# Kernel tuning notes

Hardware: AMD Instinct MI355X
Metric: run time of the kernel (lower is better)

The kernel has to match this reference:

```python
import jax, jax.numpy as jnp
import numpy as np

N = 100000   # nodes
F = 32       # input features
D = 64       # dim_inner
E = 1600000  # edges
G = 2000     # graphs
C = 10       # classes
L = 4        # GIN layers
BN_EPS = 1e-5


def _bn(h, gamma, beta):
    # training-mode BatchNorm1d over node axis (biased variance, as torch)
    mu = jnp.mean(h, axis=0)
    var = jnp.mean((h - mu) ** 2, axis=0)
    return gamma * (h - mu) * jax.lax.rsqrt(var + BN_EPS) + beta


def setup_inputs() -> dict:
    key = jax.random.key(0)
    ks = jax.random.split(key, 24)
    s = 0.05
    f32 = jnp.float32
    x = jax.random.normal(ks[0], (N, F), f32)
    edge_index = jax.random.randint(ks[1], (2, E), 0, N)
    batch_ids = jnp.sort(jax.random.randint(ks[2], (N,), 0, G))
    y = jax.random.randint(ks[3], (G,), 0, C)
    W_enc = jax.random.normal(ks[4], (F, D), f32) * s
    b_enc = jnp.zeros((D,), f32)
    W1 = jax.random.normal(ks[5], (L, D, D), f32) * s
    b1 = jnp.zeros((L, D), f32)
    g1 = jnp.ones((L, D), f32)
    be1 = jnp.zeros((L, D), f32)
    W2 = jax.random.normal(ks[6], (L, D, D), f32) * s
    b2 = jnp.zeros((L, D), f32)
    gout = jnp.ones((L, D), f32)
    bout = jnp.zeros((L, D), f32)
    fcW0 = jax.random.normal(ks[7], (F, C), f32) * s
    fcb0 = jnp.zeros((C,), f32)
    fcW = jax.random.normal(ks[8], (L, D, C), f32) * s
    fcb = jnp.zeros((L, C), f32)
    return dict(x=x, edge_index=edge_index, batch_ids=batch_ids, y=y,
                W_enc=W_enc, b_enc=b_enc, W1=W1, b1=b1, g1=g1, be1=be1,
                W2=W2, b2=b2, gout=gout, bout=bout,
                fcW0=fcW0, fcb0=fcb0, fcW=fcW, fcb=fcb)


def reference(x, edge_index, batch_ids, y, W_enc, b_enc, W1, b1, g1, be1,
              W2, b2, gout, bout, fcW0, fcb0, fcW, fcb):
    src, dst = edge_index[0], edge_index[1]
    h = x @ W_enc + b_enc  # x_encoder
    layer_outs = []
    for i in range(L):
        # GINConv, eps=0: (1+eps)*x + sum_{j->i} x_j  (scatter-add over edges)
        agg = jax.ops.segment_sum(h[src], dst, num_segments=N)
        m = h + agg
        m = jax.nn.relu(_bn(m @ W1[i] + b1[i], g1[i], be1[i]))  # MLP part 1
        m = m @ W2[i] + b2[i]                                    # MLP part 2
        h = jax.nn.relu(_bn(m, gout[i], bout[i]))                # outer BN+ReLU
        layer_outs.append(h)
    # jumping-knowledge: pooled raw features + each layer through its fc head
    out = jax.ops.segment_sum(x, batch_ids, num_segments=G) @ fcW0 + fcb0
    for i in range(L):
        pooled = jax.ops.segment_sum(layer_outs[i], batch_ids, num_segments=G)
        out = out + pooled @ fcW[i] + fcb[i]
    return (out, y)
```

## Files before the change

### kernel.cpp

```cpp
#include <hip/hip_runtime.h>


#define BN_EPS 1e-5f
#define CURS_STRIDE 16

typedef __attribute__((ext_vector_type(8))) short short8;
typedef __attribute__((ext_vector_type(4))) float f32x4;

__device__ __forceinline__ unsigned int pack_bf16x2(float a, float b) {
    unsigned int ua = __float_as_uint(a);
    unsigned int ub = __float_as_uint(b);
    ua = (ua + 0x7FFFu + ((ua >> 16) & 1u)) >> 16;
    ub = (ub + 0x7FFFu + ((ub >> 16) & 1u)) >> 16;
    return ua | (ub << 16);
}
__device__ __forceinline__ unsigned short bf16_1(float f) {
    unsigned int u = __float_as_uint(f);
    u = (u + 0x7FFFu + ((u >> 16) & 1u)) >> 16;
    return (unsigned short)u;
}
__device__ __forceinline__ float2 unpack_bf16x2(unsigned int u) {
    float2 r;
    r.x = __uint_as_float(u << 16);
    r.y = __uint_as_float(u & 0xFFFF0000u);
    return r;
}

template<bool BN>
__device__ __forceinline__ void acc_row8(float (&acc)[8], uint4 p,
                                         const float* sc, const float* sh) {
    unsigned int pp[4] = {p.x, p.y, p.z, p.w};
    #pragma unroll
    for (int t = 0; t < 4; t++) {
        float2 f = unpack_bf16x2(pp[t]);
        if (BN) {
            f.x = fmaxf(fmaf(f.x, sc[2 * t],     sh[2 * t]),     0.f);
            f.y = fmaxf(fmaf(f.y, sc[2 * t + 1], sh[2 * t + 1]), 0.f);
        }
        acc[2 * t]     += f.x;
        acc[2 * t + 1] += f.y;
    }
}

template<bool BN>
__global__ __launch_bounds__(512)
void gin_gemm1(const int* __restrict__ rowp, const int* __restrict__ srcs,
               const unsigned int* __restrict__ hb,
               const float* __restrict__ bsum, const float* __restrict__ bsumsq,
               const float* __restrict__ gamma, const float* __restrict__ beta,
               float invN,
               const float* __restrict__ W, const float* __restrict__ bias,
               unsigned short* __restrict__ out,
               float* __restrict__ stat_sum, float* __restrict__ stat_sumsq,
               int N)
{
    constexpr int AS = 72, WS = 72, KH = 2;
    __shared__ short a_lds[128 * AS];
    __shared__ short wt_lds[64 * WS];
    __shared__ float ssf[128];
    __shared__ float red[1024];

    const int tid = threadIdx.x;
    const int nb  = blockIdx.x * 128;
    const int l   = tid & 63;
    const int w   = tid >> 6;
    const int ln  = l & 15;
    const int q   = l >> 4;

    if (BN) {
        if (tid < 64) {
            float mu  = bsum[tid] * invN;
            float var = bsumsq[tid] * invN - mu * mu;
            float s   = gamma[tid] * rsqrtf(var + BN_EPS);
            ssf[tid]      = s;
            ssf[64 + tid] = beta[tid] - s * mu;
        }
        __syncthreads();
    }

    for (int idx = tid; idx < 64 * 64; idx += 512) {
        int k = idx >> 6, n = idx & 63;
        wt_lds[n * WS + k] = (short)bf16_1(W[idx]);
    }

    const uint4* hb4 = (const uint4*)hb;
    const int cc = tid & 7;
    const int rl = tid >> 3;
    float sc[8], sh[8];
    if (BN) {
        #pragma unroll
        for (int j = 0; j < 8; j++) {
            sc[j] = ssf[cc * 8 + j];
            sh[j] = ssf[64 + cc * 8 + j];
        }
    }
    for (int it = 0; it < 2; it++) {
        int rloc = it * 64 + rl;
        int n = nb + rloc;
        float acc[8] = {0.f, 0.f, 0.f, 0.f, 0.f, 0.f, 0.f, 0.f};
        if (n < N) {
            uint4 p = hb4[(size_t)n * 8 + cc];
            acc_row8<BN>(acc, p, sc, sh);
            int e = rowp[n], end = rowp[n + 1];
            for (; e + 3 < end; e += 4) {
                int a0 = srcs[e], a1 = srcs[e + 1], a2 = srcs[e + 2], a3 = srcs[e + 3];
                uint4 p0 = hb4[(size_t)a0 * 8 + cc];
                uint4 p1 = hb4[(size_t)a1 * 8 + cc];
                uint4 p2 = hb4[(size_t)a2 * 8 + cc];
                uint4 p3 = hb4[(size_t)a3 * 8 + cc];
                acc_row8<BN>(acc, p0, sc, sh);
                acc_row8<BN>(acc, p1, sc, sh);
                acc_row8<BN>(acc, p2, sc, sh);
                acc_row8<BN>(acc, p3, sc, sh);
            }
            for (; e < end; e++) {
                uint4 pp = hb4[(size_t)srcs[e] * 8 + cc];
                acc_row8<BN>(acc, pp, sc, sh);
            }
        }
        uint4 o;
        o.x = pack_bf16x2(acc[0], acc[1]);
        o.y = pack_bf16x2(acc[2], acc[3]);
        o.z = pack_bf16x2(acc[4], acc[5]);
        o.w = pack_bf16x2(acc[6], acc[7]);
        *(uint4*)&a_lds[rloc * AS + cc * 8] = o;
    }
    __syncthreads();

    short8 afrag[KH], bfrag[4][KH];
    const int rw = w * 16;
    #pragma unroll
    for (int kh = 0; kh < KH; kh++)
        afrag[kh] = *(const short8*)&a_lds[(rw + ln) * AS + kh * 32 + q * 8];
    #pragma unroll
    for (int nt = 0; nt < 4; nt++)
        #pragma unroll
        for (int kh = 0; kh < KH; kh++)
            bfrag[nt][kh] = *(const short8*)&wt_lds[(nt * 16 + ln) * WS + kh * 32 + q * 8];

    f32x4 acc[4];
    #pragma unroll
    for (int nt = 0; nt < 4; nt++) {
        float bv = bias[nt * 16 + ln];
        acc[nt] = (f32x4){bv, bv, bv, bv};
    }
    #pragma unroll
    for (int kh = 0; kh < KH; kh++)
        #pragma unroll
        for (int nt = 0; nt < 4; nt++)
            acc[nt] = __builtin_amdgcn_mfma_f32_16x16x32_bf16(
                afrag[kh], bfrag[nt][kh], acc[nt], 0, 0, 0);

    #pragma unroll
    for (int reg = 0; reg < 4; reg++) {
        int row = nb + rw + q * 4 + reg;
        if (row < N)
            #pragma unroll
            for (int nt = 0; nt < 4; nt++)
                out[(size_t)row * 64 + nt * 16 + ln] = bf16_1(acc[nt][reg]);
    }

    {
        float s1[4] = {0.f, 0.f, 0.f, 0.f};
        float s2[4] = {0.f, 0.f, 0.f, 0.f};
        #pragma unroll
        for (int reg = 0; reg < 4; reg++) {
            int row = nb + rw + q * 4 + reg;
            if (row < N)
                #pragma unroll
                for (int nt = 0; nt < 4; nt++) {
                    float v = acc[nt][reg];
                    s1[nt] += v;
                    s2[nt] += v * v;
                }
        }
        #pragma unroll
        for (int nt = 0; nt < 4; nt++) {
            s1[nt] += __shfl_xor(s1[nt], 16);
            s1[nt] += __shfl_xor(s1[nt], 32);
            s2[nt] += __shfl_xor(s2[nt], 16);
            s2[nt] += __shfl_xor(s2[nt], 32);
        }
        __syncthreads();
        if (l < 16) {
            #pragma unroll
            for (int nt = 0; nt < 4; nt++) {
                red[w * 64 + nt * 16 + l]        = s1[nt];
                red[512 + w * 64 + nt * 16 + l]  = s2[nt];
            }
        }
        __syncthreads();
        if (tid < 64) {
            float t1 = 0.f, t2 = 0.f;
            #pragma unroll
            for (int j = 0; j < 8; j++) {
                t1 += red[j * 64 + tid];
                t2 += red[512 + j * 64 + tid];
            }
            unsafeAtomicAdd(&stat_sum[tid],   t1);
            unsafeAtomicAdd(&stat_sumsq[tid], t2);
        }
    }
}

template<int K, int INK, bool STATS>
__global__ __launch_bounds__(512)
void mfma_gemm(const void* __restrict__ Av,
               const float* __restrict__ bn_sum, const float* __restrict__ bn_sumsq,
               const float* __restrict__ gamma, const float* __restrict__ beta,
               float invN,
               const float* __restrict__ W, const float* __restrict__ bias,
               unsigned short* __restrict__ out,
               float* __restrict__ stat_sum, float* __restrict__ stat_sumsq,
               int N)
{
    constexpr int AS  = K + 8;
    constexpr int WS  = K + 8;
    constexpr int CPR = K / 8;
    constexpr int KH  = K / 32;

    __shared__ short a_lds[128 * AS];
    __shared__ short wt_lds[64 * WS];
    __shared__ float ssf[128];
    __shared__ float red[1024];

    const int tid = threadIdx.x;
    const int nb  = blockIdx.x * 128;
    const int l   = tid & 63;
    const int w   = tid >> 6;
    const int ln  = l & 15;
    const int q   = l >> 4;

    if (INK == 2) {
        if (tid < 64) {
            float mu  = bn_sum[tid] * invN;
            float var = bn_sumsq[tid] * invN - mu * mu;
            float s   = gamma[tid] * rsqrtf(var + BN_EPS);
            ssf[tid]      = s;
            ssf[64 + tid] = beta[tid] - s * mu;
        }
        __syncthreads();
    }

    for (int idx = tid; idx < K * 64; idx += 512) {
        int k = idx >> 6, n = idx & 63;
        wt_lds[n * WS + k] = (short)bf16_1(W[idx]);
    }

    for (int c = tid; c < 128 * CPR; c += 512) {
        int rloc = c / CPR;
        int j    = c % CPR;
        int row  = nb + rloc;
        uint4 p = make_uint4(0u, 0u, 0u, 0u);
        if (row < N) {
            if (INK == 1) {
                const float4* xr = (const float4*)Av;
                float4 f0 = xr[(size_t)row * (K / 4) + 2 * j];
                float4 f1 = xr[(size_t)row * (K / 4) + 2 * j + 1];
                p.x = pack_bf16x2(f0.x, f0.y); p.y = pack_bf16x2(f0.z, f0.w);
                p.z = pack_bf16x2(f1.x, f1.y); p.w = pack_bf16x2(f1.z, f1.w);
            } else {
                p = ((const uint4*)Av)[(size_t)row * CPR + j];
                if (INK == 2) {
                    int k0 = j * 8;
                    unsigned int* pp = (unsigned int*)&p;
                    #pragma unroll
                    for (int t = 0; t < 4; t++) {
                        float2 f = unpack_bf16x2(pp[t]);
                        int k = k0 + 2 * t;
                        f.x = fmaxf(fmaf(f.x, ssf[k],     ssf[64 + k]),     0.f);
                        f.y = fmaxf(fmaf(f.y, ssf[k + 1], ssf[64 + k + 1]), 0.f);
                        pp[t] = pack_bf16x2(f.x, f.y);
                    }
                }
            }
        }
        *(uint4*)&a_lds[rloc * AS + j * 8] = p;
    }
    __syncthreads();

    short8 afrag[KH], bfrag[4][KH];
    const int rw = w * 16;
    #pragma unroll
    for (int kh = 0; kh < KH; kh++)
        afrag[kh] = *(const short8*)&a_lds[(rw + ln) * AS + kh * 32 + q * 8];
    #pragma unroll
    for (int nt = 0; nt < 4; nt++)
        #pragma unroll
        for (int kh = 0; kh < KH; kh++)
            bfrag[nt][kh] = *(const short8*)&wt_lds[(nt * 16 + ln) * WS + kh * 32 + q * 8];

    f32x4 acc[4];
    #pragma unroll
    for (int nt = 0; nt < 4; nt++) {
        float bv = bias[nt * 16 + ln];
        acc[nt] = (f32x4){bv, bv, bv, bv};
    }
    #pragma unroll
    for (int kh = 0; kh < KH; kh++)
        #pragma unroll
        for (int nt = 0; nt < 4; nt++)
            acc[nt] = __builtin_amdgcn_mfma_f32_16x16x32_bf16(
                afrag[kh], bfrag[nt][kh], acc[nt], 0, 0, 0);

    #pragma unroll
    for (int reg = 0; reg < 4; reg++) {
        int row = nb + rw + q * 4 + reg;
        if (row < N)
            #pragma unroll
            for (int nt = 0; nt < 4; nt++)
                out[(size_t)row * 64 + nt * 16 + ln] = bf16_1(acc[nt][reg]);
    }

    if (STATS) {
        float s1[4] = {0.f, 0.f, 0.f, 0.f};
        float s2[4] = {0.f, 0.f, 0.f, 0.f};
        #pragma unroll
        for (int reg = 0; reg < 4; reg++) {
            int row = nb + rw + q * 4 + reg;
            if (row < N)
                #pragma unroll
                for (int nt = 0; nt < 4; nt++) {
                    float v = acc[nt][reg];
                    s1[nt] += v;
                    s2[nt] += v * v;
                }
        }
        #pragma unroll
        for (int nt = 0; nt < 4; nt++) {
            s1[nt] += __shfl_xor(s1[nt], 16);
            s1[nt] += __shfl_xor(s1[nt], 32);
            s2[nt] += __shfl_xor(s2[nt], 16);
            s2[nt] += __shfl_xor(s2[nt], 32);
        }
        __syncthreads();
        if (l < 16) {
            #pragma unroll
            for (int nt = 0; nt < 4; nt++) {
                red[w * 64 + nt * 16 + l]       = s1[nt];
                red[512 + w * 64 + nt * 16 + l] = s2[nt];
            }
        }
        __syncthreads();
        if (tid < 64) {
            float t1 = 0.f, t2 = 0.f;
            #pragma unroll
            for (int j = 0; j < 8; j++) {
                t1 += red[j * 64 + tid];
                t2 += red[512 + j * 64 + tid];
            }
            unsafeAtomicAdd(&stat_sum[tid],   t1);
            unsafeAtomicAdd(&stat_sumsq[tid], t2);
        }
    }
}

__global__ __launch_bounds__(256)
void bucket_hist(const int* __restrict__ dst, int* __restrict__ bhist,
                 int E, int nb)
{
    __shared__ int lh[1024];
    for (int i = threadIdx.x; i < 1024; i += 256) lh[i] = 0;
    __syncthreads();
    for (int e = blockIdx.x * 256 + threadIdx.x; e < E; e += gridDim.x * 256)
        atomicAdd(&lh[dst[e] >> 7], 1);
    __syncthreads();
    for (int i = threadIdx.x; i < nb; i += 256)
        if (lh[i]) atomicAdd(&bhist[i], lh[i]);
}

__global__ __launch_bounds__(1024)
void bucket_scan(const int* __restrict__ bhist, int* __restrict__ bbase,
                 int* __restrict__ bcur, int nb)
{
    __shared__ int sm[1024];
    int t = threadIdx.x;
    int v = (t < nb) ? bhist[t] : 0;
    sm[t] = v; __syncthreads();
    for (int off = 1; off < 1024; off <<= 1) {
        int add = (t >= off) ? sm[t - off] : 0;
        __syncthreads();
        sm[t] += add;
        __syncthreads();
    }
    if (t <= nb) {
        int ex = sm[t] - v;
        bbase[t] = ex;
        if (t < nb) bcur[t * CURS_STRIDE] = ex;
    }
}

__global__ __launch_bounds__(256)
void bucket_scatter(const int* __restrict__ src, const int* __restrict__ dst,
                    int* __restrict__ bcur, int* __restrict__ ebuf,
                    int E, int nb)
{
    constexpr int CH = 4096;
    __shared__ int            key[CH];
    __shared__ unsigned short bid[CH];
    __shared__ int lh[800];
    __shared__ int lbase[800];

    const int t    = threadIdx.x;
    const int base = blockIdx.x * CH;
    const int cnt  = min(CH, E - base);

    for (int i = t; i < nb; i += 256) lh[i] = 0;
    __syncthreads();

    for (int i = t; i < cnt; i += 256) {
        int d = dst[base + i];
        int s = src[base + i];
        int b = d >> 7;
        key[i] = (s << 7) | (d & 127);
        bid[i] = (unsigned short)b;
        atomicAdd(&lh[b], 1);
    }
    __syncthreads();

    for (int i = t; i < nb; i += 256) {
        int c = lh[i];
        if (c) lbase[i] = atomicAdd(&bcur[i * CURS_STRIDE], c);
        lh[i] = 0;
    }
    __syncthreads();

    for (int i = t; i < cnt; i += 256) {
        int b = bid[i];
        int p = atomicAdd(&lh[b], 1);
        ebuf[lbase[b] + p] = key[i];
    }
}

__global__ __launch_bounds__(256)
void bucket_csr(const int* __restrict__ bbase, const int* __restrict__ ebuf,
                int* __restrict__ row, int* __restrict__ srcs, int N, int E)
{
    __shared__ int lh[128], lofs[128], lcur[128];
    const int b   = blockIdx.x;
    const int tid = threadIdx.x;
    const int beg = bbase[b], end = bbase[b + 1];

    if (tid < 128) lh[tid] = 0;
    __syncthreads();
    for (int e = beg + tid; e < end; e += 256)
        atomicAdd(&lh[ebuf[e] & 127], 1);
    __syncthreads();

    int v = (tid < 128) ? lh[tid] : 0;
    if (tid < 128) lofs[tid] = v;
    __syncthreads();
    for (int off = 1; off < 128; off <<= 1) {
        int add = 0;
        if (tid < 128 && tid >= off) add = lofs[tid - off];
        __syncthreads();
        if (tid < 128) lofs[tid] += add;
        __syncthreads();
    }
    if (tid < 128) {
        int ex = lofs[tid] - v;
        lcur[tid] = ex;
        int node = b * 128 + tid;
        if (node < N) row[node] = beg + ex;
    }
    if (b == 0 && tid == 0) row[N] = E;
    __syncthreads();

    for (int e = beg + tid; e < end; e += 256) {
        int pk = ebuf[e];
        int p = atomicAdd(&lcur[pk & 127], 1);
        srcs[beg + p] = pk >> 7;
    }
}

__global__ __launch_bounds__(256)
void pool_nodes(const unsigned short* __restrict__ hb,
                const float* __restrict__ bsum, const float* __restrict__ bsumsq,
                const float* __restrict__ gamma, const float* __restrict__ beta,
                float invN, const int* __restrict__ batch,
                float* __restrict__ pooled, int N)
{
    int d  = threadIdx.x & 63;
    int nl = threadIdx.x >> 6;
    int nb = blockIdx.x * 32;
    float mu  = bsum[d] * invN;
    float var = bsumsq[d] * invN - mu * mu;
    float s   = gamma[d] * rsqrtf(var + BN_EPS);
    float sh  = beta[d] - s * mu;
    float acc = 0.f;
    int cg = -1;
    #pragma unroll
    for (int r = 0; r < 8; r++) {
        int n = nb + nl * 8 + r;
        if (n >= N) break;
        int g = batch[n];
        if (g != cg) {
            if (cg >= 0) unsafeAtomicAdd(&pooled[(size_t)cg * 64 + d], acc);
            acc = 0.f; cg = g;
        }
        float v = __uint_as_float(((unsigned int)hb[(size_t)n * 64 + d]) << 16);
        acc += fmaxf(fmaf(v, s, sh), 0.f);
    }
    if (cg >= 0) unsafeAtomicAdd(&pooled[(size_t)cg * 64 + d], acc);
}

__global__ __launch_bounds__(256)
void pool_x(const float* __restrict__ x, const int* __restrict__ batch,
            float* __restrict__ px, int N)
{
    int f  = threadIdx.x & 31;
    int nl = threadIdx.x >> 5;
    int nb = blockIdx.x * 64;
    float acc = 0.f;
    int cg = -1;
    #pragma unroll
    for (int r = 0; r < 8; r++) {
        int n = nb + nl * 8 + r;
        if (n >= N) break;
        int g = batch[n];
        if (g != cg) {
            if (cg >= 0) unsafeAtomicAdd(&px[(size_t)cg * 32 + f], acc);
            acc = 0.f; cg = g;
        }
        acc += x[(size_t)n * 32 + f];
    }
    if (cg >= 0) unsafeAtomicAdd(&px[(size_t)cg * 32 + f], acc);
}

__global__ __launch_bounds__(256)
void head_kernel(const float* __restrict__ px, const float* __restrict__ pl,
                 const float* __restrict__ fcW0, const float* __restrict__ fcb0,
                 const float* __restrict__ fcW, const float* __restrict__ fcb,
                 const int* __restrict__ y, float* __restrict__ out, int G)
{
    int tid = blockIdx.x * 256 + threadIdx.x;
    int total = G * 10;
    if (tid < total) {
        int g = tid / 10, c = tid % 10;
        float acc = fcb0[c];
        const float* pxg = px + (size_t)g * 32;
        #pragma unroll
        for (int k = 0; k < 32; k++) acc = fmaf(pxg[k], fcW0[k * 10 + c], acc);
        #pragma unroll
        for (int i = 0; i < 4; i++) {
            acc += fcb[i * 10 + c];
            const float* pg = pl + ((size_t)i * G + g) * 64;
            const float* w  = fcW + i * 640;
            #pragma unroll
            for (int k = 0; k < 64; k++) acc = fmaf(pg[k], w[k * 10 + c], acc);
        }
        out[tid] = acc;
    } else if (tid < total + G) {
        out[tid] = (float)y[tid - total];
    }
}

extern "C" void kernel_launch(void* const* d_in, const int* in_sizes, int n_in,
                              void* d_out, int out_size, void* d_ws, size_t ws_size,
                              hipStream_t stream)
{
    const float* x     = (const float*)d_in[0];
    const int*   ei    = (const int*)  d_in[1];
    const int*   batch = (const int*)  d_in[2];
    const int*   y     = (const int*)  d_in[3];
    const float* W_enc = (const float*)d_in[4];
    const float* b_enc = (const float*)d_in[5];
    const float* W1    = (const float*)d_in[6];
    const float* b1    = (const float*)d_in[7];
    const float* g1    = (const float*)d_in[8];
    const float* be1   = (const float*)d_in[9];
    const float* W2    = (const float*)d_in[10];
    const float* b2    = (const float*)d_in[11];
    const float* gout  = (const float*)d_in[12];
    const float* bout  = (const float*)d_in[13];
    const float* fcW0  = (const float*)d_in[14];
    const float* fcb0  = (const float*)d_in[15];
    const float* fcW   = (const float*)d_in[16];
    const float* fcb   = (const float*)d_in[17];

    const int N = in_sizes[0] / 32;
    const int E = in_sizes[1] / 2;
    const int G = in_sizes[3];
    const int* src = ei;
    const int* dst = ei + E;
    const int NB = (N + 127) / 128;

    unsigned int* m  = (unsigned int*)d_ws;
    unsigned int* hb = m + (size_t)N * 32;
    float* stats = (float*)(hb + (size_t)N * 32);
    float* px    = stats + 1024;
    float* pl    = px + (size_t)G * 32;
    int*   row   = (int*)(pl + (size_t)4 * G * 64);
    int*   srcs  = row + (N + 1);
    int*   mi    = (int*)m;
    int*   bhist = mi;
    int*   bbase = mi + 1024;
    int*   bcur  = mi + 2048;
    int*   ebuf  = mi + 2048 + 800 * CURS_STRIDE;

    size_t zbytes = (size_t)(1024 + G * 32 + 4 * G * 64) * sizeof(float);
    hipMemsetAsync(stats, 0, zbytes, stream);
    hipMemsetAsync(bhist, 0, 1024 * sizeof(int), stream);

    bucket_hist<<<160, 256, 0, stream>>>(dst, bhist, E, NB);
    bucket_scan<<<1, 1024, 0, stream>>>(bhist, bbase, bcur, NB);
    bucket_scatter<<<(E + 4095) / 4096, 256, 0, stream>>>(src, dst, bcur, ebuf, E, NB);
    bucket_csr<<<NB, 256, 0, stream>>>(bbase, ebuf, row, srcs, N, E);

    const int gb = (N + 127) / 128;
    const float invN = 1.0f / (float)N;

    mfma_gemm<32, 1, false><<<gb, 512, 0, stream>>>(
        x, nullptr, nullptr, nullptr, nullptr, 0.f,
        W_enc, b_enc, (unsigned short*)hb, nullptr, nullptr, N);
    pool_x<<<(N + 63) / 64, 256, 0, stream>>>(x, batch, px, N);

    for (int i = 0; i < 4; i++) {
        float* s1a = stats + (i * 2 + 0) * 128;
        float* s1b = s1a + 64;
        float* s2a = stats + (i * 2 + 1) * 128;
        float* s2b = s2a + 64;

        if (i == 0) {
            gin_gemm1<false><<<gb, 512, 0, stream>>>(
                row, srcs, hb, nullptr, nullptr, nullptr, nullptr, 0.f,
                W1 + (size_t)i * 4096, b1 + i * 64, (unsigned short*)m, s1a, s1b, N);
        } else {
            float* p2a = stats + ((i - 1) * 2 + 1) * 128;
            float* p2b = p2a + 64;
            gin_gemm1<true><<<gb, 512, 0, stream>>>(
                row, srcs, hb, p2a, p2b,
                gout + (i - 1) * 64, bout + (i - 1) * 64, invN,
                W1 + (size_t)i * 4096, b1 + i * 64, (unsigned short*)m, s1a, s1b, N);
        }

        mfma_gemm<64, 2, true><<<gb, 512, 0, stream>>>(
            m, s1a, s1b, g1 + i * 64, be1 + i * 64, invN,
            W2 + (size_t)i * 4096, b2 + i * 64, (unsigned short*)hb, s2a, s2b, N);

        pool_nodes<<<(N + 31) / 32, 256, 0, stream>>>(
            (const unsigned short*)hb, s2a, s2b, gout + i * 64, bout + i * 64, invN,
            batch, pl + (size_t)i * G * 64, N);
    }

    head_kernel<<<(G * 10 + G + 255) / 256, 256, 0, stream>>>(
        px, pl, fcW0, fcb0, fcW, fcb, y, (float*)d_out, G);
}
```

Before: 564.0 us.

## Materialize BN+ReLU output in pool kernel and interleave two-row gather

The outer BatchNorm+ReLU is now applied once per node inside pool_nodes, which writes the normalized bf16 value back into hb for the next layer. The gather in gin_gemm1 therefore sums raw rows instead of redoing the affine+ReLU for every edge, and the kernel loses its BN template and LDS setup. The two rows each thread handles are gathered in an interleaved loop to keep more independent loads in flight. This adds a write pass over hb in pool_nodes and relies on the grid size gb equalling NB, which is assumed to match the 128-row block count.

```diff
diff --git a/kernel.cpp b/kernel.cpp
--- a/kernel.cpp
+++ b/kernel.cpp
@@ -26,29 +26,19 @@
     return r;
 }
 
-template<bool BN>
-__device__ __forceinline__ void acc_row8(float (&acc)[8], uint4 p,
-                                         const float* sc, const float* sh) {
+__device__ __forceinline__ void acc8(float (&acc)[8], uint4 p) {
     unsigned int pp[4] = {p.x, p.y, p.z, p.w};
     #pragma unroll
     for (int t = 0; t < 4; t++) {
         float2 f = unpack_bf16x2(pp[t]);
-        if (BN) {
-            f.x = fmaxf(fmaf(f.x, sc[2 * t],     sh[2 * t]),     0.f);
-            f.y = fmaxf(fmaf(f.y, sc[2 * t + 1], sh[2 * t + 1]), 0.f);
-        }
         acc[2 * t]     += f.x;
         acc[2 * t + 1] += f.y;
     }
 }
 
-template<bool BN>
 __global__ __launch_bounds__(512)
 void gin_gemm1(const int* __restrict__ rowp, const int* __restrict__ srcs,
-               const unsigned int* __restrict__ hb,
-               const float* __restrict__ bsum, const float* __restrict__ bsumsq,
-               const float* __restrict__ gamma, const float* __restrict__ beta,
-               float invN,
+               const unsigned int* __restrict__ tab,
                const float* __restrict__ W, const float* __restrict__ bias,
                unsigned short* __restrict__ out,
                float* __restrict__ stat_sum, float* __restrict__ stat_sumsq,
@@ -57,7 +47,6 @@
     constexpr int AS = 72, WS = 72, KH = 2;
     __shared__ short a_lds[128 * AS];
     __shared__ short wt_lds[64 * WS];
-    __shared__ float ssf[128];
     __shared__ float red[1024];
 
     const int tid = threadIdx.x;
@@ -67,63 +56,75 @@
     const int ln  = l & 15;
     const int q   = l >> 4;
 
-    if (BN) {
-        if (tid < 64) {
-            float mu  = bsum[tid] * invN;
-            float var = bsumsq[tid] * invN - mu * mu;
-            float s   = gamma[tid] * rsqrtf(var + BN_EPS);
-            ssf[tid]      = s;
-            ssf[64 + tid] = beta[tid] - s * mu;
-        }
-        __syncthreads();
-    }
-
     for (int idx = tid; idx < 64 * 64; idx += 512) {
         int k = idx >> 6, n = idx & 63;
         wt_lds[n * WS + k] = (short)bf16_1(W[idx]);
     }
 
-    const uint4* hb4 = (const uint4*)hb;
+    const uint4* tb4 = (const uint4*)tab;
     const int cc = tid & 7;
     const int rl = tid >> 3;
-    float sc[8], sh[8];
-    if (BN) {
-        #pragma unroll
-        for (int j = 0; j < 8; j++) {
-            sc[j] = ssf[cc * 8 + j];
-            sh[j] = ssf[64 + cc * 8 + j];
-        }
-    }
-    for (int it = 0; it < 2; it++) {
-        int rloc = it * 64 + rl;
-        int n = nb + rloc;
-        float acc[8] = {0.f, 0.f, 0.f, 0.f, 0.f, 0.f, 0.f, 0.f};
-        if (n < N) {
-            uint4 p = hb4[(size_t)n * 8 + cc];
-            acc_row8<BN>(acc, p, sc, sh);
-            int e = rowp[n], end = rowp[n + 1];
-            for (; e + 3 < end; e += 4) {
-                int a0 = srcs[e], a1 = srcs[e + 1], a2 = srcs[e + 2], a3 = srcs[e + 3];
-                uint4 p0 = hb4[(size_t)a0 * 8 + cc];
-                uint4 p1 = hb4[(size_t)a1 * 8 + cc];
-                uint4 p2 = hb4[(size_t)a2 * 8 + cc];
-                uint4 p3 = hb4[(size_t)a3 * 8 + cc];
-                acc_row8<BN>(acc, p0, sc, sh);
-                acc_row8<BN>(acc, p1, sc, sh);
-                acc_row8<BN>(acc, p2, sc, sh);
-                acc_row8<BN>(acc, p3, sc, sh);
-            }
-            for (; e < end; e++) {
-                uint4 pp = hb4[(size_t)srcs[e] * 8 + cc];
-                acc_row8<BN>(acc, pp, sc, sh);
-            }
-        }
+
+    float accA[8] = {0.f,0.f,0.f,0.f,0.f,0.f,0.f,0.f};
+    float accB[8] = {0.f,0.f,0.f,0.f,0.f,0.f,0.f,0.f};
+    const int nA = nb + rl;
+    const int nB = nb + 64 + rl;
+    int eA = 0, endA = 0, eB = 0, endB = 0;
+    if (nA < N) {
+        acc8(accA, tb4[(size_t)nA * 8 + cc]);
+        eA = rowp[nA]; endA = rowp[nA + 1];
+    }
+    if (nB < N) {
+        acc8(accB, tb4[(size_t)nB * 8 + cc]);
+        eB = rowp[nB]; endB = rowp[nB + 1];
+    }
+
+    while (eA + 3 < endA && eB + 3 < endB) {
+        int a0 = srcs[eA], a1 = srcs[eA+1], a2 = srcs[eA+2], a3 = srcs[eA+3];
+        int b0 = srcs[eB], b1 = srcs[eB+1], b2 = srcs[eB+2], b3 = srcs[eB+3];
+        uint4 pa0 = tb4[(size_t)a0 * 8 + cc];
+        uint4 pa1 = tb4[(size_t)a1 * 8 + cc];
+        uint4 pa2 = tb4[(size_t)a2 * 8 + cc];
+        uint4 pa3 = tb4[(size_t)a3 * 8 + cc];
+        uint4 pb0 = tb4[(size_t)b0 * 8 + cc];
+        uint4 pb1 = tb4[(size_t)b1 * 8 + cc];
+        uint4 pb2 = tb4[(size_t)b2 * 8 + cc];
+        uint4 pb3 = tb4[(size_t)b3 * 8 + cc];
+        acc8(accA, pa0); acc8(accA, pa1); acc8(accA, pa2); acc8(accA, pa3);
+        acc8(accB, pb0); acc8(accB, pb1); acc8(accB, pb2); acc8(accB, pb3);
+        eA += 4; eB += 4;
+    }
+    for (; eA + 3 < endA; eA += 4) {
+        int a0 = srcs[eA], a1 = srcs[eA+1], a2 = srcs[eA+2], a3 = srcs[eA+3];
+        uint4 p0 = tb4[(size_t)a0 * 8 + cc];
+        uint4 p1 = tb4[(size_t)a1 * 8 + cc];
+        uint4 p2 = tb4[(size_t)a2 * 8 + cc];
+        uint4 p3 = tb4[(size_t)a3 * 8 + cc];
+        acc8(accA, p0); acc8(accA, p1); acc8(accA, p2); acc8(accA, p3);
+    }
+    for (; eB + 3 < endB; eB += 4) {
+        int b0 = srcs[eB], b1 = srcs[eB+1], b2 = srcs[eB+2], b3 = srcs[eB+3];
+        uint4 p0 = tb4[(size_t)b0 * 8 + cc];
+        uint4 p1 = tb4[(size_t)b1 * 8 + cc];
+        uint4 p2 = tb4[(size_t)b2 * 8 + cc];
+        uint4 p3 = tb4[(size_t)b3 * 8 + cc];
+        acc8(accB, p0); acc8(accB, p1); acc8(accB, p2); acc8(accB, p3);
+    }
+    for (; eA < endA; eA++) acc8(accA, tb4[(size_t)srcs[eA] * 8 + cc]);
+    for (; eB < endB; eB++) acc8(accB, tb4[(size_t)srcs[eB] * 8 + cc]);
+
+    {
         uint4 o;
-        o.x = pack_bf16x2(acc[0], acc[1]);
-        o.y = pack_bf16x2(acc[2], acc[3]);
-        o.z = pack_bf16x2(acc[4], acc[5]);
-        o.w = pack_bf16x2(acc[6], acc[7]);
-        *(uint4*)&a_lds[rloc * AS + cc * 8] = o;
+        o.x = pack_bf16x2(accA[0], accA[1]);
+        o.y = pack_bf16x2(accA[2], accA[3]);
+        o.z = pack_bf16x2(accA[4], accA[5]);
+        o.w = pack_bf16x2(accA[6], accA[7]);
+        *(uint4*)&a_lds[rl * AS + cc * 8] = o;
+        o.x = pack_bf16x2(accB[0], accB[1]);
+        o.y = pack_bf16x2(accB[2], accB[3]);
+        o.z = pack_bf16x2(accB[4], accB[5]);
+        o.w = pack_bf16x2(accB[6], accB[7]);
+        *(uint4*)&a_lds[(64 + rl) * AS + cc * 8] = o;
     }
     __syncthreads();
 
@@ -474,11 +475,11 @@
 }
 
 __global__ __launch_bounds__(256)
-void pool_nodes(const unsigned short* __restrict__ hb,
+void pool_nodes(unsigned short* __restrict__ hb,
                 const float* __restrict__ bsum, const float* __restrict__ bsumsq,
                 const float* __restrict__ gamma, const float* __restrict__ beta,
                 float invN, const int* __restrict__ batch,
-                float* __restrict__ pooled, int N)
+                float* __restrict__ pooled, int N, int writeT)
 {
     int d  = threadIdx.x & 63;
     int nl = threadIdx.x >> 6;
@@ -499,7 +500,9 @@
             acc = 0.f; cg = g;
         }
         float v = __uint_as_float(((unsigned int)hb[(size_t)n * 64 + d]) << 16);
-        acc += fmaxf(fmaf(v, s, sh), 0.f);
+        float t = fmaxf(fmaf(v, s, sh), 0.f);
+        if (writeT) hb[(size_t)n * 64 + d] = bf16_1(t);
+        acc += t;
     }
     if (cg >= 0) unsafeAtomicAdd(&pooled[(size_t)cg * 64 + d], acc);
 }
@@ -607,7 +610,7 @@
     bucket_scatter<<<(E + 4095) / 4096, 256, 0, stream>>>(src, dst, bcur, ebuf, E, NB);
     bucket_csr<<<NB, 256, 0, stream>>>(bbase, ebuf, row, srcs, N, E);
 
-    const int gb = (N + 127) / 128;
+    const int gb = NB;
     const float invN = 1.0f / (float)N;
 
     mfma_gemm<32, 1, false><<<gb, 512, 0, stream>>>(
@@ -621,26 +624,17 @@
         float* s2a = stats + (i * 2 + 1) * 128;
         float* s2b = s2a + 64;
 
-        if (i == 0) {
-            gin_gemm1<false><<<gb, 512, 0, stream>>>(
-                row, srcs, hb, nullptr, nullptr, nullptr, nullptr, 0.f,
-                W1 + (size_t)i * 4096, b1 + i * 64, (unsigned short*)m, s1a, s1b, N);
-        } else {
-            float* p2a = stats + ((i - 1) * 2 + 1) * 128;
-            float* p2b = p2a + 64;
-            gin_gemm1<true><<<gb, 512, 0, stream>>>(
-                row, srcs, hb, p2a, p2b,
-                gout + (i - 1) * 64, bout + (i - 1) * 64, invN,
-                W1 + (size_t)i * 4096, b1 + i * 64, (unsigned short*)m, s1a, s1b, N);
-        }
+        gin_gemm1<<<gb, 512, 0, stream>>>(
+            row, srcs, hb,
+            W1 + (size_t)i * 4096, b1 + i * 64, (unsigned short*)m, s1a, s1b, N);
 
         mfma_gemm<64, 2, true><<<gb, 512, 0, stream>>>(
             m, s1a, s1b, g1 + i * 64, be1 + i * 64, invN,
             W2 + (size_t)i * 4096, b2 + i * 64, (unsigned short*)hb, s2a, s2b, N);
 
         pool_nodes<<<(N + 31) / 32, 256, 0, stream>>>(
-            (const unsigned short*)hb, s2a, s2b, gout + i * 64, bout + i * 64, invN,
-            batch, pl + (size_t)i * G * 64, N);
+            (unsigned short*)hb, s2a, s2b, gout + i * 64, bout + i * 64, invN,
+            batch, pl + (size_t)i * G * 64, N, (i < 3) ? 1 : 0);
     }
 
     head_kernel<<<(G * 10 + G + 255) / 256, 256, 0, stream>>>(
```

After: 585.3 us. +3.8%, slower.
